# Performance work log

Measured on AMD Instinct MI355X. Metric: run time of the kernel, lower is better.

Reference implementation:

```python
import jax, jax.numpy as jnp
import numpy as np

B, S, HID = 2, 2048, 3072
H, HKV, D = 16, 8, 256
ROPE_THETA = 10000.0
NEG_INF = -1e9


def setup_inputs() -> dict:
    key = jax.random.key(0)
    ks = jax.random.split(key, 5)
    hidden_states = jax.random.normal(ks[0], (B, S, HID), jnp.float32)
    # rotary frequencies: complex freqs_cis = cos + i*sin, shape (B, S, D//2)
    inv_freq = 1.0 / (ROPE_THETA ** (np.arange(0, D, 2, dtype=np.float32) / D))
    ang = np.arange(S, dtype=np.float32)[:, None] * inv_freq[None, :]  # (S, D//2)
    cos = jnp.asarray(np.broadcast_to(np.cos(ang)[None], (B, S, D // 2)).copy())
    sin = jnp.asarray(np.broadcast_to(np.sin(ang)[None], (B, S, D // 2)).copy())
    causal = jnp.tril(jnp.ones((S, S), dtype=bool))
    mask = jnp.where(causal, 0.0, NEG_INF).astype(jnp.float32)[None, None]  # (1,1,S,S)
    wq = jax.random.normal(ks[1], (HID, H * D), jnp.float32) * 0.02
    wk = jax.random.normal(ks[2], (HID, HKV * D), jnp.float32) * 0.02
    wv = jax.random.normal(ks[3], (HID, HKV * D), jnp.float32) * 0.02
    wo = jax.random.normal(ks[4], (H * D, HID), jnp.float32) * 0.02
    return {"hidden_states": hidden_states, "cos": cos, "sin": sin, "mask": mask,
            "wq": wq, "wk": wk, "wv": wv, "wo": wo}


def _apply_rotary(x, cos, sin):
    # x: (B, S, Hx, D). Torch code forms complex pairs (x[..., :D/2], x[..., D/2:])
    # and multiplies by freqs_cis = cos + i*sin, then re-concats real||imag halves.
    half = x.shape[-1] // 2
    x1, x2 = x[..., :half], x[..., half:]
    c = cos[:, :, None, :]  # (B, S, 1, D/2)
    s = sin[:, :, None, :]
    return jnp.concatenate([x1 * c - x2 * s, x1 * s + x2 * c], axis=-1)


def reference(hidden_states, cos, sin, mask, wq, wk, wv, wo):
    b, s, _ = hidden_states.shape
    q = (hidden_states @ wq).reshape(b, s, H, D)
    k = (hidden_states @ wk).reshape(b, s, HKV, D)
    v = (hidden_states @ wv).reshape(b, s, HKV, D)
    q = _apply_rotary(q, cos, sin)
    k = _apply_rotary(k, cos, sin)
    # GQA: group query heads per kv head instead of materializing repeated K/V
    g = H // HKV
    qg = q.reshape(b, s, HKV, g, D)
    scaling = D ** (-0.5)
    scores = jnp.einsum('bskgd,btkd->bkgst', qg, k) * scaling  # (B,HKV,G,S,S)
    scores = scores + mask[:, :, None]  # broadcast (1,1,1,S,S)
    probs = jax.nn.softmax(scores, axis=-1)
    out = jnp.einsum('bkgst,btkd->bskgd', probs, v).reshape(b, s, H * D)
    return out @ wo
```

## Files before the change

### kernel.cpp

```cpp
#include <hip/hip_runtime.h>

typedef short bf16x8 __attribute__((ext_vector_type(8)));
typedef float f32x4 __attribute__((ext_vector_type(4)));

#define S_LEN 2048
#define NHQ 16
#define NKV 8
#define HD 256

__device__ __forceinline__ unsigned short f2bf(float f){
  unsigned u = __float_as_uint(f);
  unsigned r = (u + 0x7FFFu + ((u >> 16) & 1u)) >> 16;
  return (unsigned short)r;
}
__device__ __forceinline__ float bf2f(unsigned short h){
  return __uint_as_float(((unsigned)h) << 16);
}
__device__ __forceinline__ unsigned pack2(float a, float b){
  return (unsigned)f2bf(a) | ((unsigned)f2bf(b) << 16);
}

__global__ void k_conv(const float* __restrict__ in, unsigned short* __restrict__ out, int n){
  int i = (blockIdx.x * 256 + threadIdx.x) * 4;
  if (i < n){
    float4 v = *(const float4*)&in[i];
    ushort4 o;
    o.x = f2bf(v.x); o.y = f2bf(v.y); o.z = f2bf(v.z); o.w = f2bf(v.w);
    *(ushort4*)&out[i] = o;
  }
}

__global__ void k_tconv(const float* __restrict__ in, unsigned short* __restrict__ out, int R, int C){
  __shared__ float tile[32][33];
  int c0 = blockIdx.x * 32, r0 = blockIdx.y * 32;
  int tx = threadIdx.x, ty = threadIdx.y;
  for (int i = 0; i < 4; i++)
    tile[ty + i*8][tx] = in[(size_t)(r0 + ty + i*8) * C + c0 + tx];
  __syncthreads();
  for (int i = 0; i < 4; i++)
    out[(size_t)(c0 + ty + i*8) * R + r0 + tx] = f2bf(tile[tx][ty + i*8]);
}

__global__ void k_vtrans(const unsigned short* __restrict__ V, unsigned short* __restrict__ VT){
  __shared__ unsigned short tile[32][40];
  int s0 = blockIdx.x * 32, d0 = blockIdx.y * 32, bz = blockIdx.z;
  int b = bz >> 3, kv = bz & 7;
  int tx = threadIdx.x, ty = threadIdx.y;
  for (int i = 0; i < 4; i++)
    tile[ty + i*8][tx] = V[(size_t)(b * S_LEN + s0 + ty + i*8) * (NKV*HD) + kv*HD + d0 + tx];
  __syncthreads();
  for (int i = 0; i < 4; i++)
    VT[((size_t)(bz * HD + d0 + ty + i*8)) * S_LEN + s0 + tx] = tile[tx][ty + i*8];
}

__global__ void k_rope(unsigned short* buf, const float* __restrict__ cosb,
                       const float* __restrict__ sinb, int lgnh){
  int idx = blockIdx.x * 256 + threadIdx.x;
  int d = idx & 127;
  int h = (idx >> 7) & ((1 << lgnh) - 1);
  int t = idx >> (7 + lgnh);
  float c = cosb[t * 128 + d], s = sinb[t * 128 + d];
  size_t base = ((size_t)t << (lgnh + 8)) + ((size_t)h << 8) + d;
  float x1 = bf2f(buf[base]), x2 = bf2f(buf[base + 128]);
  buf[base]       = f2bf(x1 * c - x2 * s);
  buf[base + 128] = f2bf(x1 * s + x2 * c);
}

__global__ __launch_bounds__(256) void k_gemm_bt(const unsigned short* __restrict__ A,
    const unsigned short* __restrict__ Bt, void* __restrict__ Cp,
    int M, int N, int K, int out_bf16){
  __shared__ __align__(16) unsigned short smem[2 * 128 * 64];
  unsigned short* As = smem;
  unsigned short* Bs = smem + 128 * 64;
  int tid = threadIdx.x;
  int lane = tid & 63, wave = tid >> 6, quad = lane >> 4, l16 = lane & 15;
  int wm = wave >> 1, wn = wave & 1;
  int bm0 = blockIdx.y * 128, bn0 = blockIdx.x * 128;
  f32x4 acc[4][4] = {};
  for (int k0 = 0; k0 < K; k0 += 64){
    __syncthreads();
    for (int it = 0; it < 4; it++){
      int slot = it * 256 + tid;
      int row = slot >> 3, c = slot & 7;
      int pc = c ^ (row & 7);
      *(uint4*)&As[row * 64 + pc * 8] = *(const uint4*)&A[(size_t)(bm0 + row) * K + k0 + c * 8];
      *(uint4*)&Bs[row * 64 + pc * 8] = *(const uint4*)&Bt[(size_t)(bn0 + row) * K + k0 + c * 8];
    }
    __syncthreads();
    for (int ks = 0; ks < 2; ks++){
      bf16x8 af[4], bfr[4];
      for (int mt = 0; mt < 4; mt++){
        int row = wm * 64 + mt * 16 + l16;
        int pc = (ks * 4 + quad) ^ (row & 7);
        af[mt] = *(const bf16x8*)&As[row * 64 + pc * 8];
      }
      for (int nt = 0; nt < 4; nt++){
        int row = wn * 64 + nt * 16 + l16;
        int pc = (ks * 4 + quad) ^ (row & 7);
        bfr[nt] = *(const bf16x8*)&Bs[row * 64 + pc * 8];
      }
      for (int mt = 0; mt < 4; mt++)
        for (int nt = 0; nt < 4; nt++)
          acc[mt][nt] = __builtin_amdgcn_mfma_f32_16x16x32_bf16(af[mt], bfr[nt], acc[mt][nt], 0, 0, 0);
    }
  }
  float* Ct = (float*)smem;
  for (int p = 0; p < 2; p++){
    __syncthreads();
    if (wm == p){
      for (int mt = 0; mt < 4; mt++)
        for (int nt = 0; nt < 4; nt++)
          for (int r = 0; r < 4; r++)
            Ct[(mt * 16 + quad * 4 + r) * 128 + wn * 64 + nt * 16 + l16] = acc[mt][nt][r];
    }
    __syncthreads();
    if (out_bf16){
      unsigned short* O = (unsigned short*)Cp;
      for (int j = 0; j < 4; j++){
        int chunk = j * 256 + tid;
        int row = chunk >> 4, col = (chunk & 15) * 8;
        const float* src = &Ct[row * 128 + col];
        uint4 o;
        o.x = pack2(src[0], src[1]);
        o.y = pack2(src[2], src[3]);
        o.z = pack2(src[4], src[5]);
        o.w = pack2(src[6], src[7]);
        *(uint4*)&O[(size_t)(bm0 + p * 64 + row) * N + bn0 + col] = o;
      }
    } else {
      float* O = (float*)Cp;
      for (int j = 0; j < 8; j++){
        int chunk = j * 256 + tid;
        int row = chunk >> 5, col = (chunk & 31) * 4;
        *(float4*)&O[(size_t)(bm0 + p * 64 + row) * N + bn0 + col] = *(const float4*)&Ct[row * 128 + col];
      }
    }
  }
}

__global__ __launch_bounds__(512, 2) void k_flash(const unsigned short* __restrict__ Q,
    const unsigned short* __restrict__ Kg, const unsigned short* __restrict__ VTg,
    unsigned short* __restrict__ Og){
  __shared__ __align__(16) unsigned short smem[2 * (32*264 + 256*40) + 8 * 16 * 40];
  const int BUFSZ = 32*264 + 256*40;
  int tid = threadIdx.x;
  int lane = tid & 63, wave = tid >> 6, quad = lane >> 4, l16 = lane & 15;
  int hig = wave & 1, rowgrp = wave >> 1;
  int bkv = blockIdx.x, p = blockIdx.y;
  int b = bkv >> 3, kv = bkv & 7;
  int h = kv * 2 + hig;
  const float L2E = 1.4426950408889634f;
  const float scale = 0.0625f;

  size_t kgbase = (size_t)(b * S_LEN) * (NKV*HD) + (size_t)kv * HD;
  size_t vtbase = ((size_t)(b * NKV + kv) * HD) * S_LEN;
  unsigned short* Ps = smem + 2 * BUFSZ + wave * (16 * 40);

  for (int ph = 0; ph < 2; ph++){
    int qt = ph ? (31 - p) : p;
    int qmin = qt * 64 + rowgrp * 16;
    int nkt = qt * 2 + 2;

    bf16x8 qf[8];
    {
      size_t qoff = ((size_t)(b * S_LEN + qt * 64 + rowgrp * 16 + l16)) * (NHQ * HD) + (size_t)h * HD;
      for (int ks = 0; ks < 8; ks++)
        qf[ks] = *(const bf16x8*)&Q[qoff + ks * 32 + quad * 8];
    }
    f32x4 acc[16] = {};
    float mrow[4], lrow[4];
    for (int r = 0; r < 4; r++){ mrow[r] = -1e30f; lrow[r] = 0.f; }

    uint4 stk[2], stv[2];
    for (int it = 0; it < 2; it++){
      int slot = it * 512 + tid;
      int kr = slot >> 5, c = slot & 31;
      stk[it] = *(const uint4*)&Kg[kgbase + (size_t)(kr) * (NKV*HD) + c * 8];
      int dd = slot >> 2, c2 = slot & 3;
      stv[it] = *(const uint4*)&VTg[vtbase + (size_t)dd * S_LEN + c2 * 8];
    }

    for (int kt = 0; kt < nkt; kt++){
      unsigned short* Ks  = smem + (kt & 1) * BUFSZ;
      unsigned short* VTs = Ks + 32 * 264;
      for (int it = 0; it < 2; it++){
        int slot = it * 512 + tid;
        int kr = slot >> 5, c = slot & 31;
        *(uint4*)&Ks[kr * 264 + c * 8] = stk[it];
        int dd = slot >> 2, c2 = slot & 3;
        *(uint4*)&VTs[dd * 40 + c2 * 8] = stv[it];
      }
      if (kt + 1 < nkt){
        for (int it = 0; it < 2; it++){
          int slot = it * 512 + tid;
          int kr = slot >> 5, c = slot & 31;
          stk[it] = *(const uint4*)&Kg[kgbase + (size_t)((kt + 1) * 32 + kr) * (NKV*HD) + c * 8];
          int dd = slot >> 2, c2 = slot & 3;
          stv[it] = *(const uint4*)&VTg[vtbase + (size_t)dd * S_LEN + (kt + 1) * 32 + c2 * 8];
        }
      }
      __syncthreads();
      if (kt * 32 > qmin + 15) continue;

      f32x4 sv[2] = {};
      __builtin_amdgcn_s_setprio(1);
      for (int ks = 0; ks < 8; ks++){
        for (int nt = 0; nt < 2; nt++){
          bf16x8 kf = *(const bf16x8*)&Ks[(nt * 16 + l16) * 264 + ks * 32 + quad * 8];
          sv[nt] = __builtin_amdgcn_mfma_f32_16x16x32_bf16(qf[ks], kf, sv[nt], 0, 0, 0);
        }
      }
      __builtin_amdgcn_s_setprio(0);
      float pv[2][4], tmax[4];
      for (int r = 0; r < 4; r++){
        int qr = qmin + quad * 4 + r;
        float mx = -1e30f;
        for (int nt = 0; nt < 2; nt++){
          int key = kt * 32 + nt * 16 + l16;
          float v = sv[nt][r] * scale;
          if (key > qr) v = -1e30f;
          pv[nt][r] = v;
          mx = fmaxf(mx, v);
        }
        tmax[r] = mx;
      }
      for (int off = 1; off < 16; off <<= 1)
        for (int r = 0; r < 4; r++)
          tmax[r] = fmaxf(tmax[r], __shfl_xor(tmax[r], off, 64));
      int grow = (tmax[0] > mrow[0]) | (tmax[1] > mrow[1]) |
                 (tmax[2] > mrow[2]) | (tmax[3] > mrow[3]);
      if (grow){
        float alpha[4];
        for (int r = 0; r < 4; r++){
          float mn = fmaxf(mrow[r], tmax[r]);
          alpha[r] = exp2f((mrow[r] - mn) * L2E);
          mrow[r] = mn;
          lrow[r] *= alpha[r];
        }
        for (int i = 0; i < 16; i++)
          for (int r = 0; r < 4; r++) acc[i][r] *= alpha[r];
      }
      float pb[2][4], psum[4] = {0.f, 0.f, 0.f, 0.f};
      for (int nt = 0; nt < 2; nt++)
        for (int r = 0; r < 4; r++){
          float pe = exp2f((pv[nt][r] - mrow[r]) * L2E);
          pb[nt][r] = pe; psum[r] += pe;
        }
      for (int off = 1; off < 16; off <<= 1)
        for (int r = 0; r < 4; r++)
          psum[r] += __shfl_xor(psum[r], off, 64);
      for (int r = 0; r < 4; r++) lrow[r] += psum[r];
      for (int nt = 0; nt < 2; nt++)
        for (int r = 0; r < 4; r++)
          Ps[(quad * 4 + r) * 40 + nt * 16 + l16] = f2bf(pb[nt][r]);
      bf16x8 pa = *(const bf16x8*)&Ps[l16 * 40 + quad * 8];
      __builtin_amdgcn_s_setprio(1);
      for (int nt = 0; nt < 16; nt++){
        bf16x8 vf = *(const bf16x8*)&VTs[(nt * 16 + l16) * 40 + quad * 8];
        acc[nt] = __builtin_amdgcn_mfma_f32_16x16x32_bf16(pa, vf, acc[nt], 0, 0, 0);
      }
      __builtin_amdgcn_s_setprio(0);
    }
    float inv[4];
    for (int r = 0; r < 4; r++) inv[r] = 1.0f / lrow[r];
    __syncthreads();
    unsigned short* Ot = smem + wave * (16 * 256);
    for (int nt = 0; nt < 16; nt++)
      for (int r = 0; r < 4; r++)
        Ot[(quad * 4 + r) * 256 + nt * 16 + l16] = f2bf(acc[nt][r] * inv[r]);
    size_t obase = ((size_t)(b * S_LEN + qt * 64 + rowgrp * 16)) * (NHQ * HD) + (size_t)h * HD;
    for (int j = 0; j < 8; j++){
      int chunk = j * 64 + lane;
      int row = chunk >> 5, col = (chunk & 31) * 8;
      *(uint4*)&Og[obase + (size_t)row * (NHQ * HD) + col] = *(const uint4*)&Ot[row * 256 + col];
    }
    __syncthreads();
  }
}

extern "C" void kernel_launch(void* const* d_in, const int* in_sizes, int n_in,
                              void* d_out, int out_size, void* d_ws, size_t ws_size,
                              hipStream_t stream){
  const float* hid  = (const float*)d_in[0];
  const float* cosb = (const float*)d_in[1];
  const float* sinb = (const float*)d_in[2];
  const float* wq = (const float*)d_in[4];
  const float* wk = (const float*)d_in[5];
  const float* wv = (const float*)d_in[6];
  const float* wo = (const float*)d_in[7];

  char* ws = (char*)d_ws;
  size_t off = 0;
  auto alloc = [&](size_t bytes) -> void* {
    void* p = ws + off; off += (bytes + 255) & ~(size_t)255; return p;
  };
  unsigned short* Xbf = (unsigned short*)alloc(4096ull * 3072 * 2);
  unsigned short* WqT = (unsigned short*)alloc(4096ull * 3072 * 2);
  unsigned short* WkT = (unsigned short*)alloc(2048ull * 3072 * 2);
  unsigned short* WvT = (unsigned short*)alloc(2048ull * 3072 * 2);
  unsigned short* WoT = (unsigned short*)alloc(3072ull * 4096 * 2);
  unsigned short* Qb  = (unsigned short*)alloc(4096ull * 4096 * 2);
  unsigned short* Kb  = (unsigned short*)alloc(4096ull * 2048 * 2);
  unsigned short* Vb  = (unsigned short*)alloc(4096ull * 2048 * 2);
  unsigned short* VTb = (unsigned short*)alloc(4096ull * 2048 * 2);
  unsigned short* Ab  = (unsigned short*)alloc(4096ull * 4096 * 2);

  k_conv<<<12288, 256, 0, stream>>>(hid, Xbf, 4096 * 3072);
  k_tconv<<<dim3(128, 96), dim3(32, 8), 0, stream>>>(wq, WqT, 3072, 4096);
  k_tconv<<<dim3(64, 96),  dim3(32, 8), 0, stream>>>(wk, WkT, 3072, 2048);
  k_tconv<<<dim3(64, 96),  dim3(32, 8), 0, stream>>>(wv, WvT, 3072, 2048);
  k_tconv<<<dim3(96, 128), dim3(32, 8), 0, stream>>>(wo, WoT, 4096, 3072);
  k_gemm_bt<<<dim3(32, 32), 256, 0, stream>>>(Xbf, WqT, Qb, 4096, 4096, 3072, 1);
  k_gemm_bt<<<dim3(16, 32), 256, 0, stream>>>(Xbf, WkT, Kb, 4096, 2048, 3072, 1);
  k_gemm_bt<<<dim3(16, 32), 256, 0, stream>>>(Xbf, WvT, Vb, 4096, 2048, 3072, 1);
  k_rope<<<32768, 256, 0, stream>>>(Qb, cosb, sinb, 4);
  k_rope<<<16384, 256, 0, stream>>>(Kb, cosb, sinb, 3);
  k_vtrans<<<dim3(64, 8, 16), dim3(32, 8), 0, stream>>>(Vb, VTb);
  k_flash<<<dim3(16, 16), 512, 0, stream>>>(Qb, Kb, VTb, Ab);
  k_gemm_bt<<<dim3(24, 32), 256, 0, stream>>>(Ab, WoT, d_out, 4096, 3072, 4096, 0);
}
```

Baseline: 900.7 us.

## Read K/V fragments directly from global memory in flash attention, dropping LDS staging

Removes the block-wide double-buffered LDS staging of K and V^T tiles and the per-tile __syncthreads. Each wave now loads its MFMA operand fragments straight from global (relying on L1/L2 caching) and runs its own causal trip count. The aim is to cut barrier stalls and LDS traffic and let waves progress independently. In exchange there is more redundant global/L2 traffic, since several waves reload the same K/V, and no software prefetch to hide load latency.

```diff
diff --git a/kernel.cpp b/kernel.cpp
--- a/kernel.cpp
+++ b/kernel.cpp
@@ -141,8 +141,7 @@
 __global__ __launch_bounds__(512, 2) void k_flash(const unsigned short* __restrict__ Q,
     const unsigned short* __restrict__ Kg, const unsigned short* __restrict__ VTg,
     unsigned short* __restrict__ Og){
-  __shared__ __align__(16) unsigned short smem[2 * (32*264 + 256*40) + 8 * 16 * 40];
-  const int BUFSZ = 32*264 + 256*40;
+  __shared__ __align__(16) unsigned short smem[8 * 16 * 256];
   int tid = threadIdx.x;
   int lane = tid & 63, wave = tid >> 6, quad = lane >> 4, l16 = lane & 15;
   int hig = wave & 1, rowgrp = wave >> 1;
@@ -152,18 +151,19 @@
   const float L2E = 1.4426950408889634f;
   const float scale = 0.0625f;
 
-  size_t kgbase = (size_t)(b * S_LEN) * (NKV*HD) + (size_t)kv * HD;
-  size_t vtbase = ((size_t)(b * NKV + kv) * HD) * S_LEN;
-  unsigned short* Ps = smem + 2 * BUFSZ + wave * (16 * 40);
+  const unsigned short* Kbase = Kg + (size_t)(b * S_LEN) * (NKV*HD) + (size_t)kv * HD;
+  const unsigned short* Vbase = VTg + (size_t)(bkv * HD) * S_LEN;
+  unsigned short* Ps = smem + wave * 4096;
+  unsigned short* Ot = smem + wave * 4096;
 
   for (int ph = 0; ph < 2; ph++){
     int qt = ph ? (31 - p) : p;
     int qmin = qt * 64 + rowgrp * 16;
-    int nkt = qt * 2 + 2;
+    int nkt = (qmin + 15) / 32 + 1;
 
     bf16x8 qf[8];
     {
-      size_t qoff = ((size_t)(b * S_LEN + qt * 64 + rowgrp * 16 + l16)) * (NHQ * HD) + (size_t)h * HD;
+      size_t qoff = ((size_t)(b * S_LEN + qmin + l16)) * (NHQ * HD) + (size_t)h * HD;
       for (int ks = 0; ks < 8; ks++)
         qf[ks] = *(const bf16x8*)&Q[qoff + ks * 32 + quad * 8];
     }
@@ -171,42 +171,15 @@
     float mrow[4], lrow[4];
     for (int r = 0; r < 4; r++){ mrow[r] = -1e30f; lrow[r] = 0.f; }
 
-    uint4 stk[2], stv[2];
-    for (int it = 0; it < 2; it++){
-      int slot = it * 512 + tid;
-      int kr = slot >> 5, c = slot & 31;
-      stk[it] = *(const uint4*)&Kg[kgbase + (size_t)(kr) * (NKV*HD) + c * 8];
-      int dd = slot >> 2, c2 = slot & 3;
-      stv[it] = *(const uint4*)&VTg[vtbase + (size_t)dd * S_LEN + c2 * 8];
-    }
-
     for (int kt = 0; kt < nkt; kt++){
-      unsigned short* Ks  = smem + (kt & 1) * BUFSZ;
-      unsigned short* VTs = Ks + 32 * 264;
-      for (int it = 0; it < 2; it++){
-        int slot = it * 512 + tid;
-        int kr = slot >> 5, c = slot & 31;
-        *(uint4*)&Ks[kr * 264 + c * 8] = stk[it];
-        int dd = slot >> 2, c2 = slot & 3;
-        *(uint4*)&VTs[dd * 40 + c2 * 8] = stv[it];
-      }
-      if (kt + 1 < nkt){
-        for (int it = 0; it < 2; it++){
-          int slot = it * 512 + tid;
-          int kr = slot >> 5, c = slot & 31;
-          stk[it] = *(const uint4*)&Kg[kgbase + (size_t)((kt + 1) * 32 + kr) * (NKV*HD) + c * 8];
-          int dd = slot >> 2, c2 = slot & 3;
-          stv[it] = *(const uint4*)&VTg[vtbase + (size_t)dd * S_LEN + (kt + 1) * 32 + c2 * 8];
-        }
-      }
-      __syncthreads();
-      if (kt * 32 > qmin + 15) continue;
+      const unsigned short* Kt = Kbase + (size_t)(kt * 32) * (NKV*HD);
+      const unsigned short* Vt = Vbase + kt * 32;
 
       f32x4 sv[2] = {};
       __builtin_amdgcn_s_setprio(1);
       for (int ks = 0; ks < 8; ks++){
         for (int nt = 0; nt < 2; nt++){
-          bf16x8 kf = *(const bf16x8*)&Ks[(nt * 16 + l16) * 264 + ks * 32 + quad * 8];
+          bf16x8 kf = *(const bf16x8*)&Kt[(size_t)(nt * 16 + l16) * (NKV*HD) + ks * 32 + quad * 8];
           sv[nt] = __builtin_amdgcn_mfma_f32_16x16x32_bf16(qf[ks], kf, sv[nt], 0, 0, 0);
         }
       }
@@ -256,25 +229,22 @@
       bf16x8 pa = *(const bf16x8*)&Ps[l16 * 40 + quad * 8];
       __builtin_amdgcn_s_setprio(1);
       for (int nt = 0; nt < 16; nt++){
-        bf16x8 vf = *(const bf16x8*)&VTs[(nt * 16 + l16) * 40 + quad * 8];
+        bf16x8 vf = *(const bf16x8*)&Vt[(size_t)(nt * 16 + l16) * S_LEN + quad * 8];
         acc[nt] = __builtin_amdgcn_mfma_f32_16x16x32_bf16(pa, vf, acc[nt], 0, 0, 0);
       }
       __builtin_amdgcn_s_setprio(0);
     }
     float inv[4];
     for (int r = 0; r < 4; r++) inv[r] = 1.0f / lrow[r];
-    __syncthreads();
-    unsigned short* Ot = smem + wave * (16 * 256);
     for (int nt = 0; nt < 16; nt++)
       for (int r = 0; r < 4; r++)
         Ot[(quad * 4 + r) * 256 + nt * 16 + l16] = f2bf(acc[nt][r] * inv[r]);
-    size_t obase = ((size_t)(b * S_LEN + qt * 64 + rowgrp * 16)) * (NHQ * HD) + (size_t)h * HD;
+    size_t obase = ((size_t)(b * S_LEN + qmin)) * (NHQ * HD) + (size_t)h * HD;
     for (int j = 0; j < 8; j++){
       int chunk = j * 64 + lane;
       int row = chunk >> 5, col = (chunk & 31) * 8;
       *(uint4*)&Og[obase + (size_t)row * (NHQ * HD) + col] = *(const uint4*)&Ot[row * 256 + col];
     }
-    __syncthreads();
   }
 }
 
```

Measured after the change: 1.149 ms. 27.5% more time.
